# Optimization experiments

Hardware: AMD Instinct MI355X
Metric: run time of the kernel (lower is better)

The kernel has to match this reference:

```python
import jax, jax.numpy as jnp
import numpy as np

D_MODEL = 1024
SCALE = float(np.sqrt(D_MODEL))


def setup_inputs() -> dict:
    key = jax.random.key(0)
    k1, k2, k3 = jax.random.split(key, 3)
    input_data = jax.random.normal(k1, (4, 2048, D_MODEL), dtype=jnp.float32)
    qk = jax.random.normal(k2, (D_MODEL, D_MODEL), dtype=jnp.float32) / SCALE
    ov = jax.random.normal(k3, (D_MODEL, D_MODEL), dtype=jnp.float32) / SCALE
    return {"input_data": input_data, "qk": qk, "ov": ov}


def reference(input_data, qk, ov):
    # input_data: [B, S, D]; qk, ov: [D, D]
    S = input_data.shape[1]
    # scores: [B, S, S] = (x @ qk) @ x^T / sqrt(D)
    scores = jnp.einsum("bsd,de,bte->bst", input_data, qk, input_data) / SCALE
    # causal mask: positions t > s get -inf (upper triangle, diagonal=1)
    causal = jnp.tril(jnp.ones((S, S), dtype=bool))
    scores = jnp.where(causal, scores, -jnp.inf)
    attn = jax.nn.softmax(scores, axis=-1)
    # A: [B, S, D] = attn @ x @ ov
    return jnp.einsum("bst,btd,de->bse", attn, input_data, ov)
```

## Files before the change

### kernel.cpp

```cpp
#include <hip/hip_runtime.h>
#include <hip/hip_bf16.h>
#include <cstdint>
#include <cstddef>
#include <type_traits>


using bf16 = __hip_bfloat16;
typedef __attribute__((ext_vector_type(8))) short short8;
typedef __attribute__((ext_vector_type(4))) float f32x4;

#define NB 4
#define SS 2048
#define DD 1024

__device__ __forceinline__ void async_lds16(const bf16* g, bf16* l) {
  __builtin_amdgcn_global_load_lds(
      (const __attribute__((address_space(1))) void*)g,
      (__attribute__((address_space(3))) void*)l,
      16, 0, 0);
}

struct alignas(8) bf16x4s { bf16 a, b, c, d; };

__global__ __launch_bounds__(256) void prep_kernel(const float* __restrict__ x,
                                                   bf16* __restrict__ xb,
                                                   const float* __restrict__ qk,
                                                   bf16* __restrict__ qkT,
                                                   const float* __restrict__ ov,
                                                   bf16* __restrict__ ovT,
                                                   float* __restrict__ l) {
  __shared__ bf16 tile[64][65];
  const int bx = blockIdx.x;
  if (bx < 8192) {
    int i = (bx * 256 + threadIdx.x) * 4;
    float4 v = *(const float4*)(x + i);
    bf16x4s o{__float2bfloat16(v.x), __float2bfloat16(v.y),
              __float2bfloat16(v.z), __float2bfloat16(v.w)};
    *(bf16x4s*)(xb + i) = o;
  } else if (bx < 8704) {
    const int idx = bx - 8192;
    const float* in = (idx & 256) ? ov : qk;
    bf16* out = (idx & 256) ? ovT : qkT;
    const int rem = idx & 255;
    const int tbx = (rem & 15) * 64;
    const int tby = (rem >> 4) * 64;
    const int tc = threadIdx.x & 63;
    const int tr = threadIdx.x >> 6;
#pragma unroll
    for (int r = tr; r < 64; r += 4)
      tile[tc][r] = __float2bfloat16(in[(size_t)(tby + r) * DD + tbx + tc]);
    __syncthreads();
#pragma unroll
    for (int r = tr; r < 64; r += 4)
      out[(size_t)(tbx + r) * DD + tby + tc] = tile[r][tc];
  } else {
    const int t = (bx - 8704) * 256 + threadIdx.x;
    f32x4 z = {0.f, 0.f, 0.f, 0.f};
    *(f32x4*)(l + t * 4) = z;
  }
}

__device__ __forceinline__ void gemm256_core(const bf16* __restrict__ Ab,
                                             const bf16* __restrict__ Bb,
                                             bf16* __restrict__ C,
                                             int N, int K, int m0, int n0, int nk,
                                             bf16* As, bf16* Bs) {
  const int lane = threadIdx.x & 63;
  const int wave = threadIdx.x >> 6;
  const int wr   = wave >> 2;
  const int wc   = wave & 3;
  const int quad = lane >> 4;
  const int r    = lane & 15;

  f32x4 acc[8][4];
#pragma unroll
  for (int i = 0; i < 8; ++i)
#pragma unroll
    for (int n = 0; n < 4; ++n) acc[i][n] = f32x4{0.f, 0.f, 0.f, 0.f};

  const int lrow = lane >> 3;
  const int lsw  = (lane & 7) ^ lrow;
  const long long a_lane = (long long)(m0 + wave * 8 + lrow) * K + lsw * 8;
  const long long b_lane = (long long)(n0 + wave * 8 + lrow) * K + lsw * 8;

  auto stageA = [&](int kt, int rnd, int buf) {
    async_lds16(Ab + a_lane + (long long)(rnd * 64) * K + (long long)kt * 64,
                As + buf * 16384 + (rnd * 64 + wave * 8) * 64);
  };
  auto stageB = [&](int kt, int rnd, int buf) {
    async_lds16(Bb + b_lane + (long long)(rnd * 64) * K + (long long)kt * 64,
                Bs + buf * 16384 + (rnd * 64 + wave * 8) * 64);
  };

  stageA(0, 0, 0); stageA(0, 2, 0);
  stageB(0, 0, 0); stageB(0, 1, 0); stageB(0, 2, 0); stageB(0, 3, 0);
  stageA(0, 1, 0); stageA(0, 3, 0);
  asm volatile("s_waitcnt vmcnt(2)" ::: "memory");
  asm volatile("s_barrier" ::: "memory");

  const int ca0 = (quad ^ (r & 7)) * 8;
  const int ca1 = ((4 + quad) ^ (r & 7)) * 8;

  for (int kt = 0; kt < nk; ++kt) {
    const int buf = kt & 1, nxt = buf ^ 1;
    const bool hn = (kt + 1 < nk);
    const bf16* Abuf = As + buf * 16384 + (wr * 128) * 64;
    const bf16* Bbuf = Bs + buf * 16384 + (wc * 64) * 64;

    auto phase = [&](auto RHC, int ca, auto&& stg, int wmode) {
      constexpr int RH = decltype(RHC)::value;
      short8 af[4], bfr[4];
#pragma unroll
      for (int m = 0; m < 4; ++m)
        af[m] = *(const short8*)(Abuf + (RH * 64 + m * 16 + r) * 64 + ca);
#pragma unroll
      for (int n = 0; n < 4; ++n)
        bfr[n] = *(const short8*)(Bbuf + (n * 16 + r) * 64 + ca);
      stg();
      asm volatile("s_barrier" ::: "memory");
      asm volatile("s_waitcnt lgkmcnt(0)" ::: "memory");
      __builtin_amdgcn_sched_barrier(0);
      __builtin_amdgcn_s_setprio(1);
#pragma unroll
      for (int m = 0; m < 4; ++m)
#pragma unroll
        for (int n = 0; n < 4; ++n)
          acc[RH * 4 + m][n] = __builtin_amdgcn_mfma_f32_16x16x32_bf16(
              af[m], bfr[n], acc[RH * 4 + m][n], 0, 0, 0);
      __builtin_amdgcn_s_setprio(0);
      if (wmode == 1) {
        if (hn) asm volatile("s_waitcnt vmcnt(2)" ::: "memory");
        else    asm volatile("s_waitcnt vmcnt(0)" ::: "memory");
      } else if (wmode == 2) {
        if (hn) asm volatile("s_waitcnt vmcnt(2)" ::: "memory");
      }
      asm volatile("s_barrier" ::: "memory");
    };

    phase(std::integral_constant<int, 0>{}, ca0,
          [&] { if (hn) { stageA(kt + 1, 0, nxt); stageA(kt + 1, 2, nxt); } }, 1);
    phase(std::integral_constant<int, 1>{}, ca0,
          [&] { if (hn) { stageB(kt + 1, 0, nxt); stageB(kt + 1, 1, nxt); } }, 0);
    phase(std::integral_constant<int, 0>{}, ca1,
          [&] { if (hn) { stageB(kt + 1, 2, nxt); stageB(kt + 1, 3, nxt); } }, 0);
    phase(std::integral_constant<int, 1>{}, ca1,
          [&] { if (hn) { stageA(kt + 1, 1, nxt); stageA(kt + 1, 3, nxt); } }, 2);
  }

#pragma unroll
  for (int i = 0; i < 8; ++i) {
    const int row0 = m0 + wr * 128 + i * 16 + quad * 4;
#pragma unroll
    for (int n = 0; n < 4; ++n) {
      const int col = n0 + wc * 64 + n * 16 + r;
#pragma unroll
      for (int q = 0; q < 4; ++q)
        C[(long long)(row0 + q) * N + col] = __float2bfloat16(acc[i][n][q]);
    }
  }
}

__global__ __launch_bounds__(512, 2) void gemm_qv256(const bf16* __restrict__ xb,
                                                     const bf16* __restrict__ qkT,
                                                     const bf16* __restrict__ ovT,
                                                     bf16* __restrict__ Qb,
                                                     bf16* __restrict__ Vt) {
  extern __shared__ bf16 lds[];
  bf16* As = lds;
  bf16* Bs = lds + 32768;
  const long long SD = (long long)SS * DD;
  const int z = blockIdx.z;
  if (z < 4) {
    const int bn = blockIdx.x & 3, bm = blockIdx.x >> 2;
    gemm256_core(xb + z * SD, qkT, Qb + z * SD, DD, DD, bm * 256, bn * 256, 16, As, Bs);
  } else {
    const int bm = blockIdx.x & 3, bn = blockIdx.x >> 2;
    gemm256_core(ovT, xb + (z - 4) * SD, Vt + (z - 4) * SD, SS, DD, bm * 256, bn * 256, 16, As, Bs);
  }
}

template <int EPI, int STAGES>
__device__ __forceinline__ void gemm_core(const bf16* __restrict__ Ab,
                                          const bf16* __restrict__ Bb,
                                          void* __restrict__ C,
                                          int N, int K, int m0, int n0, int nk,
                                          bf16* As, bf16* Bs,
                                          float* __restrict__ l) {
  const int tid  = threadIdx.x;
  const int lane = tid & 63;
  const int wave = tid >> 6;
  const int wm   = (wave >> 1) << 6;
  const int wn   = (wave & 1) << 6;
  const int quad = lane >> 4;
  const int r    = lane & 15;

  f32x4 zero = {0.f, 0.f, 0.f, 0.f};
  f32x4 acc[4][4];
#pragma unroll
  for (int i = 0; i < 4; ++i)
#pragma unroll
    for (int j = 0; j < 4; ++j) acc[i][j] = zero;

  const long long aoff = (long long)(m0 + (tid >> 2)) * K + (tid & 3) * 8;
  const long long boff = (long long)(n0 + (tid >> 2)) * K + (tid & 3) * 8;

  auto stage = [&](int kt, int s) {
    const long long k0 = (long long)kt << 5;
    bf16* lA = As + s * 4096 + wave * 512;
    bf16* lB = Bs + s * 4096 + wave * 512;
    async_lds16(Ab + aoff + k0, lA);
    async_lds16(Ab + aoff + 64LL * K + k0, lA + 2048);
    async_lds16(Bb + boff + k0, lB);
    async_lds16(Bb + boff + 64LL * K + k0, lB + 2048);
  };

  stage(0, 0);
  if (STAGES == 3 && nk > 1) stage(1, 1);

  int s = 0;
  for (int kt = 0; kt < nk; ++kt) {
    if (STAGES == 3) {
      if (kt + 2 < nk) {
        int s2 = s + 2; if (s2 >= 3) s2 -= 3;
        stage(kt + 2, s2);
        asm volatile("s_waitcnt vmcnt(8)" ::: "memory");
      } else if (kt + 1 < nk) {
        asm volatile("s_waitcnt vmcnt(4)" ::: "memory");
      } else {
        asm volatile("s_waitcnt vmcnt(0)" ::: "memory");
      }
    } else {
      if (kt + 1 < nk) {
        stage(kt + 1, s ^ 1);
        asm volatile("s_waitcnt vmcnt(4)" ::: "memory");
      } else {
        asm volatile("s_waitcnt vmcnt(0)" ::: "memory");
      }
    }
    asm volatile("s_barrier" ::: "memory");

    const bf16* Ak = As + s * 4096;
    const bf16* Bk = Bs + s * 4096;
    short8 af[4], bfr[4];
#pragma unroll
    for (int i = 0; i < 4; ++i)
      af[i] = *(const short8*)(Ak + (wm + i * 16 + r) * 32 + quad * 8);
#pragma unroll
    for (int i = 0; i < 4; ++i)
      bfr[i] = *(const short8*)(Bk + (wn + i * 16 + r) * 32 + quad * 8);
#pragma unroll
    for (int i = 0; i < 4; ++i)
#pragma unroll
      for (int j = 0; j < 4; ++j)
        acc[i][j] = __builtin_amdgcn_mfma_f32_16x16x32_bf16(af[i], bfr[j], acc[i][j], 0, 0, 0);

    asm volatile("s_barrier" ::: "memory");
    if (STAGES == 3) { if (++s == 3) s = 0; } else { s ^= 1; }
  }

#pragma unroll
  for (int i = 0; i < 4; ++i) {
    const int row0 = m0 + wm + i * 16 + quad * 4;
    if (EPI == 2) {
      float qs[4] = {0.f, 0.f, 0.f, 0.f};
#pragma unroll
      for (int j = 0; j < 4; ++j) {
        const int col = n0 + wn + j * 16 + r;
#pragma unroll
        for (int q = 0; q < 4; ++q) {
          const int row = row0 + q;
          float v = (col <= row) ? __expf(acc[i][j][q] * 0.03125f) : 0.0f;
          ((bf16*)C)[(long long)row * N + col] = __float2bfloat16(v);
          qs[q] += v;
        }
      }
#pragma unroll
      for (int q = 0; q < 4; ++q) {
#pragma unroll
        for (int off = 1; off < 16; off <<= 1) qs[q] += __shfl_xor(qs[q], off, 64);
        if (r == 0) atomicAdd(&l[row0 + q], qs[q]);
      }
    } else {
      float rs[4];
#pragma unroll
      for (int q = 0; q < 4; ++q) rs[q] = 1.0f / l[row0 + q];
#pragma unroll
      for (int j = 0; j < 4; ++j) {
        const int col = n0 + wn + j * 16 + r;
#pragma unroll
        for (int q = 0; q < 4; ++q)
          ((float*)C)[(long long)(row0 + q) * N + col] = acc[i][j][q] * rs[q];
      }
    }
  }
}

__global__ __launch_bounds__(256) void gemm_sc(const bf16* __restrict__ Qb,
                                               const bf16* __restrict__ xb,
                                               bf16* __restrict__ P,
                                               float* __restrict__ l) {
  __shared__ bf16 As[2 * 4096];
  __shared__ bf16 Bs[2 * 4096];
  const long long SD = (long long)SS * DD;
  const long long SSQ = (long long)SS * SS;
  const int t = blockIdx.x;
  int bm = (int)((sqrtf(8.0f * (float)t + 1.0f) - 1.0f) * 0.5f);
  while ((bm + 1) * (bm + 2) / 2 <= t) ++bm;
  while (bm * (bm + 1) / 2 > t) --bm;
  const int bn = t - bm * (bm + 1) / 2;
  const int b = blockIdx.z;
  gemm_core<2, 2>(Qb + b * SD, xb + b * SD, P + b * SSQ, SS, DD, bm * 128, bn * 128, 32,
                  As, Bs, l + b * SS);
}

__global__ __launch_bounds__(256) void gemm_pv(const bf16* __restrict__ P,
                                               const bf16* __restrict__ Vt,
                                               const float* __restrict__ l,
                                               float* __restrict__ out) {
  __shared__ bf16 As[2 * 4096];
  __shared__ bf16 Bs[2 * 4096];
  const long long SD = (long long)SS * DD;
  const long long SSQ = (long long)SS * SS;
  const int bm = 15 - blockIdx.y;
  const int m0 = bm * 128;
  const int nk = (m0 + 128) >> 5;
  const int b = blockIdx.z;
  gemm_core<3, 2>(P + b * SSQ, Vt + b * SD, out + b * SD, DD, SS, m0, blockIdx.x * 128, nk,
                  As, Bs, (float*)l + b * SS);
}

extern "C" void kernel_launch(void* const* d_in, const int* in_sizes, int n_in,
                              void* d_out, int out_size, void* d_ws, size_t ws_size,
                              hipStream_t stream) {
  const float* x  = (const float*)d_in[0];
  const float* qk = (const float*)d_in[1];
  const float* ov = (const float*)d_in[2];
  float* out = (float*)d_out;

  char* ws = (char*)d_ws;
  const size_t MB = 1ull << 20;
  bf16*  xb  = (bf16*)(ws + 0);
  bf16*  qkT = (bf16*)(ws + 16 * MB);
  bf16*  ovT = (bf16*)(ws + 18 * MB);
  bf16*  Qb  = (bf16*)(ws + 20 * MB);
  bf16*  Vt  = (bf16*)(ws + 36 * MB);
  bf16*  P   = (bf16*)(ws + 52 * MB);
  float* l   = (float*)(ws + 84 * MB);

  static bool lds_opt_in = false;
  if (!lds_opt_in) {
    hipFuncSetAttribute((const void*)gemm_qv256,
                        hipFuncAttributeMaxDynamicSharedMemorySize, 131072);
    lds_opt_in = true;
  }

  prep_kernel<<<dim3(8712), 256, 0, stream>>>(x, xb, qk, qkT, ov, ovT, l);
  gemm_qv256<<<dim3(32, 1, 8), 512, 131072, stream>>>(xb, qkT, ovT, Qb, Vt);
  gemm_sc<<<dim3(136, 1, 4), 256, 0, stream>>>(Qb, xb, P, l);
  gemm_pv<<<dim3(8, 16, 4), 256, 0, stream>>>(P, Vt, l, out);
}
```

Before: 219.3 us.

## Use 256x256 pipelined GEMM core for causal score and PV kernels

```diff
diff --git a/kernel.cpp b/kernel.cpp
--- a/kernel.cpp
+++ b/kernel.cpp
@@ -60,11 +60,13 @@
   }
 }
 
+template <int EPI>
 __device__ __forceinline__ void gemm256_core(const bf16* __restrict__ Ab,
                                              const bf16* __restrict__ Bb,
-                                             bf16* __restrict__ C,
+                                             void* __restrict__ C,
                                              int N, int K, int m0, int n0, int nk,
-                                             bf16* As, bf16* Bs) {
+                                             bf16* As, bf16* Bs,
+                                             float* __restrict__ l) {
   const int lane = threadIdx.x & 63;
   const int wave = threadIdx.x >> 6;
   const int wr   = wave >> 2;
@@ -150,12 +152,44 @@
 #pragma unroll
   for (int i = 0; i < 8; ++i) {
     const int row0 = m0 + wr * 128 + i * 16 + quad * 4;
-#pragma unroll
-    for (int n = 0; n < 4; ++n) {
-      const int col = n0 + wc * 64 + n * 16 + r;
-#pragma unroll
-      for (int q = 0; q < 4; ++q)
-        C[(long long)(row0 + q) * N + col] = __float2bfloat16(acc[i][n][q]);
+    if (EPI == 1) {
+#pragma unroll
+      for (int n = 0; n < 4; ++n) {
+        const int col = n0 + wc * 64 + n * 16 + r;
+#pragma unroll
+        for (int q = 0; q < 4; ++q)
+          ((bf16*)C)[(long long)(row0 + q) * N + col] = __float2bfloat16(acc[i][n][q]);
+      }
+    } else if (EPI == 2) {
+      float qs[4] = {0.f, 0.f, 0.f, 0.f};
+#pragma unroll
+      for (int n = 0; n < 4; ++n) {
+        const int col = n0 + wc * 64 + n * 16 + r;
+#pragma unroll
+        for (int q = 0; q < 4; ++q) {
+          const int row = row0 + q;
+          float v = (col <= row) ? __expf(acc[i][n][q] * 0.03125f) : 0.0f;
+          ((bf16*)C)[(long long)row * N + col] = __float2bfloat16(v);
+          qs[q] += v;
+        }
+      }
+#pragma unroll
+      for (int q = 0; q < 4; ++q) {
+#pragma unroll
+        for (int off = 1; off < 16; off <<= 1) qs[q] += __shfl_xor(qs[q], off, 64);
+        if (r == 0) atomicAdd(&l[row0 + q], qs[q]);
+      }
+    } else {
+      float rs[4];
+#pragma unroll
+      for (int q = 0; q < 4; ++q) rs[q] = 1.0f / l[row0 + q];
+#pragma unroll
+      for (int n = 0; n < 4; ++n) {
+        const int col = n0 + wc * 64 + n * 16 + r;
+#pragma unroll
+        for (int q = 0; q < 4; ++q)
+          ((float*)C)[(long long)(row0 + q) * N + col] = acc[i][n][q] * rs[q];
+      }
     }
   }
 }
@@ -172,135 +206,22 @@
   const int z = blockIdx.z;
   if (z < 4) {
     const int bn = blockIdx.x & 3, bm = blockIdx.x >> 2;
-    gemm256_core(xb + z * SD, qkT, Qb + z * SD, DD, DD, bm * 256, bn * 256, 16, As, Bs);
+    gemm256_core<1>(xb + z * SD, qkT, Qb + z * SD, DD, DD, bm * 256, bn * 256, 16,
+                    As, Bs, nullptr);
   } else {
     const int bm = blockIdx.x & 3, bn = blockIdx.x >> 2;
-    gemm256_core(ovT, xb + (z - 4) * SD, Vt + (z - 4) * SD, SS, DD, bm * 256, bn * 256, 16, As, Bs);
-  }
-}
-
-template <int EPI, int STAGES>
-__device__ __forceinline__ void gemm_core(const bf16* __restrict__ Ab,
-                                          const bf16* __restrict__ Bb,
-                                          void* __restrict__ C,
-                                          int N, int K, int m0, int n0, int nk,
-                                          bf16* As, bf16* Bs,
-                                          float* __restrict__ l) {
-  const int tid  = threadIdx.x;
-  const int lane = tid & 63;
-  const int wave = tid >> 6;
-  const int wm   = (wave >> 1) << 6;
-  const int wn   = (wave & 1) << 6;
-  const int quad = lane >> 4;
-  const int r    = lane & 15;
-
-  f32x4 zero = {0.f, 0.f, 0.f, 0.f};
-  f32x4 acc[4][4];
-#pragma unroll
-  for (int i = 0; i < 4; ++i)
-#pragma unroll
-    for (int j = 0; j < 4; ++j) acc[i][j] = zero;
-
-  const long long aoff = (long long)(m0 + (tid >> 2)) * K + (tid & 3) * 8;
-  const long long boff = (long long)(n0 + (tid >> 2)) * K + (tid & 3) * 8;
-
-  auto stage = [&](int kt, int s) {
-    const long long k0 = (long long)kt << 5;
-    bf16* lA = As + s * 4096 + wave * 512;
-    bf16* lB = Bs + s * 4096 + wave * 512;
-    async_lds16(Ab + aoff + k0, lA);
-    async_lds16(Ab + aoff + 64LL * K + k0, lA + 2048);
-    async_lds16(Bb + boff + k0, lB);
-    async_lds16(Bb + boff + 64LL * K + k0, lB + 2048);
-  };
-
-  stage(0, 0);
-  if (STAGES == 3 && nk > 1) stage(1, 1);
-
-  int s = 0;
-  for (int kt = 0; kt < nk; ++kt) {
-    if (STAGES == 3) {
-      if (kt + 2 < nk) {
-        int s2 = s + 2; if (s2 >= 3) s2 -= 3;
-        stage(kt + 2, s2);
-        asm volatile("s_waitcnt vmcnt(8)" ::: "memory");
-      } else if (kt + 1 < nk) {
-        asm volatile("s_waitcnt vmcnt(4)" ::: "memory");
-      } else {
-        asm volatile("s_waitcnt vmcnt(0)" ::: "memory");
-      }
-    } else {
-      if (kt + 1 < nk) {
-        stage(kt + 1, s ^ 1);
-        asm volatile("s_waitcnt vmcnt(4)" ::: "memory");
-      } else {
-        asm volatile("s_waitcnt vmcnt(0)" ::: "memory");
-      }
-    }
-    asm volatile("s_barrier" ::: "memory");
-
-    const bf16* Ak = As + s * 4096;
-    const bf16* Bk = Bs + s * 4096;
-    short8 af[4], bfr[4];
-#pragma unroll
-    for (int i = 0; i < 4; ++i)
-      af[i] = *(const short8*)(Ak + (wm + i * 16 + r) * 32 + quad * 8);
-#pragma unroll
-    for (int i = 0; i < 4; ++i)
-      bfr[i] = *(const short8*)(Bk + (wn + i * 16 + r) * 32 + quad * 8);
-#pragma unroll
-    for (int i = 0; i < 4; ++i)
-#pragma unroll
-      for (int j = 0; j < 4; ++j)
-        acc[i][j] = __builtin_amdgcn_mfma_f32_16x16x32_bf16(af[i], bfr[j], acc[i][j], 0, 0, 0);
-
-    asm volatile("s_barrier" ::: "memory");
-    if (STAGES == 3) { if (++s == 3) s = 0; } else { s ^= 1; }
-  }
-
-#pragma unroll
-  for (int i = 0; i < 4; ++i) {
-    const int row0 = m0 + wm + i * 16 + quad * 4;
-    if (EPI == 2) {
-      float qs[4] = {0.f, 0.f, 0.f, 0.f};
-#pragma unroll
-      for (int j = 0; j < 4; ++j) {
-        const int col = n0 + wn + j * 16 + r;
-#pragma unroll
-        for (int q = 0; q < 4; ++q) {
-          const int row = row0 + q;
-          float v = (col <= row) ? __expf(acc[i][j][q] * 0.03125f) : 0.0f;
-          ((bf16*)C)[(long long)row * N + col] = __float2bfloat16(v);
-          qs[q] += v;
-        }
-      }
-#pragma unroll
-      for (int q = 0; q < 4; ++q) {
-#pragma unroll
-        for (int off = 1; off < 16; off <<= 1) qs[q] += __shfl_xor(qs[q], off, 64);
-        if (r == 0) atomicAdd(&l[row0 + q], qs[q]);
-      }
-    } else {
-      float rs[4];
-#pragma unroll
-      for (int q = 0; q < 4; ++q) rs[q] = 1.0f / l[row0 + q];
-#pragma unroll
-      for (int j = 0; j < 4; ++j) {
-        const int col = n0 + wn + j * 16 + r;
-#pragma unroll
-        for (int q = 0; q < 4; ++q)
-          ((float*)C)[(long long)(row0 + q) * N + col] = acc[i][j][q] * rs[q];
-      }
-    }
-  }
-}
-
-__global__ __launch_bounds__(256) void gemm_sc(const bf16* __restrict__ Qb,
-                                               const bf16* __restrict__ xb,
-                                               bf16* __restrict__ P,
-                                               float* __restrict__ l) {
-  __shared__ bf16 As[2 * 4096];
-  __shared__ bf16 Bs[2 * 4096];
+    gemm256_core<1>(ovT, xb + (z - 4) * SD, Vt + (z - 4) * SD, SS, DD, bm * 256, bn * 256, 16,
+                    As, Bs, nullptr);
+  }
+}
+
+__global__ __launch_bounds__(512, 2) void gemm_sc256(const bf16* __restrict__ Qb,
+                                                     const bf16* __restrict__ xb,
+                                                     bf16* __restrict__ P,
+                                                     float* __restrict__ l) {
+  extern __shared__ bf16 lds[];
+  bf16* As = lds;
+  bf16* Bs = lds + 32768;
   const long long SD = (long long)SS * DD;
   const long long SSQ = (long long)SS * SS;
   const int t = blockIdx.x;
@@ -309,24 +230,24 @@
   while (bm * (bm + 1) / 2 > t) --bm;
   const int bn = t - bm * (bm + 1) / 2;
   const int b = blockIdx.z;
-  gemm_core<2, 2>(Qb + b * SD, xb + b * SD, P + b * SSQ, SS, DD, bm * 128, bn * 128, 32,
+  gemm256_core<2>(Qb + b * SD, xb + b * SD, P + b * SSQ, SS, DD, bm * 256, bn * 256, 16,
                   As, Bs, l + b * SS);
 }
 
-__global__ __launch_bounds__(256) void gemm_pv(const bf16* __restrict__ P,
-                                               const bf16* __restrict__ Vt,
-                                               const float* __restrict__ l,
-                                               float* __restrict__ out) {
-  __shared__ bf16 As[2 * 4096];
-  __shared__ bf16 Bs[2 * 4096];
+__global__ __launch_bounds__(512, 2) void gemm_pv256(const bf16* __restrict__ P,
+                                                     const bf16* __restrict__ Vt,
+                                                     const float* __restrict__ l,
+                                                     float* __restrict__ out) {
+  extern __shared__ bf16 lds[];
+  bf16* As = lds;
+  bf16* Bs = lds + 32768;
   const long long SD = (long long)SS * DD;
   const long long SSQ = (long long)SS * SS;
-  const int bm = 15 - blockIdx.y;
-  const int m0 = bm * 128;
-  const int nk = (m0 + 128) >> 5;
+  const int bx = blockIdx.x & 3;
+  const int bm = blockIdx.x >> 2;
   const int b = blockIdx.z;
-  gemm_core<3, 2>(P + b * SSQ, Vt + b * SD, out + b * SD, DD, SS, m0, blockIdx.x * 128, nk,
-                  As, Bs, (float*)l + b * SS);
+  gemm256_core<3>(P + b * SSQ, Vt + b * SD, out + b * SD, DD, SS,
+                  bm * 256, bx * 256, 4 * (bm + 1), As, Bs, (float*)l + b * SS);
 }
 
 extern "C" void kernel_launch(void* const* d_in, const int* in_sizes, int n_in,
@@ -351,11 +272,15 @@
   if (!lds_opt_in) {
     hipFuncSetAttribute((const void*)gemm_qv256,
                         hipFuncAttributeMaxDynamicSharedMemorySize, 131072);
+    hipFuncSetAttribute((const void*)gemm_sc256,
+                        hipFuncAttributeMaxDynamicSharedMemorySize, 131072);
+    hipFuncSetAttribute((const void*)gemm_pv256,
+                        hipFuncAttributeMaxDynamicSharedMemorySize, 131072);
     lds_opt_in = true;
   }
 
   prep_kernel<<<dim3(8712), 256, 0, stream>>>(x, xb, qk, qkT, ov, ovT, l);
   gemm_qv256<<<dim3(32, 1, 8), 512, 131072, stream>>>(xb, qkT, ovT, Qb, Vt);
-  gemm_sc<<<dim3(136, 1, 4), 256, 0, stream>>>(Qb, xb, P, l);
-  gemm_pv<<<dim3(8, 16, 4), 256, 0, stream>>>(P, Vt, l, out);
-}
+  gemm_sc256<<<dim3(36, 1, 4), 512, 131072, stream>>>(Qb, xb, P, l);
+  gemm_pv256<<<dim3(32, 1, 4), 512, 131072, stream>>>(P, Vt, l, out);
+}
```

Result: no change. 217.0 us (-1.0%).
